# Kernel optimization log

Measured on AMD Instinct MI355X. Metric: run time of the kernel, lower is better.

The kernel has to match this reference:

```python
import jax, jax.numpy as jnp
import numpy as np

N, L, A, C, C2 = 10000, 5, 6, 20, 20

def setup_inputs() -> dict:
    key = jax.random.key(0)
    k1, k2, k3, k4 = jax.random.split(key, 4)
    stats = jax.random.uniform(k1, (N, L, A, C2), dtype=jnp.float32)
    layerS = jax.random.uniform(k2, (L,), dtype=jnp.float32)
    layerS = layerS / layerS.sum()
    arcS = jax.random.uniform(k3, (L, A), dtype=jnp.float32)
    arcS = arcS / arcS.sum(axis=1, keepdims=True)
    transition = jax.random.uniform(k4, (L, A, C, C2), dtype=jnp.float32)
    transition = transition / transition.sum(axis=2, keepdims=True)  # columns over C sum to 1
    return {"stats": stats, "layerS": layerS, "arcS": arcS, "transition": transition}

def reference(stats, layerS, arcS, transition):
    # neighbDim: [N,L,A,1,1]; zeros replaced by 1 to avoid div-by-zero
    neighbDim = stats.sum(axis=3, keepdims=True)[..., None]
    neighbDim = jnp.where(neighbDim == 0, jnp.float32(1.0), neighbDim)
    # rightmost_term: [N,L,A,C,C2]
    rightmost_term = transition[None, :, :, :, :] * stats[:, :, :, None, :] / neighbDim
    # tmp: [N,L,C] = sum over arcs of arcS * sum_{C2} rightmost
    tmp = (arcS[None, :, :, None] * rightmost_term.sum(axis=4)).sum(axis=2)
    # p_Q_given_obs: [N,C]
    p_Q_given_obs = (layerS[None, :, None] * tmp).sum(axis=1)
    # transition_posterior: [N,L,A,C,C2]
    transition_posterior = (layerS[None, :, None, None, None]
                            * arcS[None, :, :, None, None]
                            * rightmost_term)
    return (p_Q_given_obs, transition_posterior, rightmost_term)
```

## Files before the change

kernel.cpp:

```cpp
#include <hip/hip_runtime.h>
#include <hip/hip_bf16.h>


#define PQ_COUNT   200000
#define POST_OFF   200000
#define RT_OFF     (200000 + 120000000)

__global__ __launch_bounds__(256) void cgmm_kernel(
    const float* __restrict__ stats,
    const float* __restrict__ layerS,
    const float* __restrict__ arcS,
    const float* __restrict__ T,
    float* __restrict__ out)
{
    __shared__ __attribute__((aligned(16))) float s[600];
    __shared__ float invb[30];
    __shared__ float wgt[30];
    __shared__ float red[200];

    const int n = blockIdx.x;
    const int t = threadIdx.x;

    const float* sn = stats + (size_t)n * 600;
    for (int i = t; i < 600; i += 256) s[i] = sn[i];
    __syncthreads();

    if (t < 30) {
        float sum = 0.f;
        #pragma unroll
        for (int j = 0; j < 20; ++j) sum += s[t * 20 + j];
        invb[t] = (sum == 0.f) ? 1.f : 1.f / sum;
        wgt[t]  = layerS[t / 6] * arcS[t];
    }
    __syncthreads();

    const float4* T4 = (const float4*)T;
    const float4* s4 = (const float4*)s;
    float4* post4 = (float4*)(out + POST_OFF) + (size_t)n * 3000;
    float4* rt4o  = (float4*)(out + RT_OFF)   + (size_t)n * 3000;

    float acc = 0.f;
    if (t < 200) {
        const int r = t % 100;
        const int q = r % 5;
        #pragma unroll
        for (int pb = 0; pb < 30; pb += 2) {
            const int p = pb + t / 100;
            const float inv = invb[p];
            const float w   = wgt[p];
            const float4 tv = T4[p * 100 + r];
            const float4 sv = s4[p * 5 + q];
            float4 rt;
            rt.x = tv.x * sv.x * inv;
            rt.y = tv.y * sv.y * inv;
            rt.z = tv.z * sv.z * inv;
            rt.w = tv.w * sv.w * inv;
            float4 po;
            po.x = rt.x * w; po.y = rt.y * w;
            po.z = rt.z * w; po.w = rt.w * w;
            rt4o [p * 100 + r] = rt;
            post4[p * 100 + r] = po;
            acc += po.x + po.y + po.z + po.w;
        }
        red[t] = acc;
    }
    __syncthreads();

    if (t < 20) {
        float pq = 0.f;
        #pragma unroll
        for (int k = 0; k < 5; ++k)
            pq += red[t * 5 + k] + red[100 + t * 5 + k];
        out[(size_t)n * 20 + t] = pq;
    }
}

extern "C" void kernel_launch(void* const* d_in, const int* in_sizes, int n_in,
                              void* d_out, int out_size, void* d_ws, size_t ws_size,
                              hipStream_t stream) {
    const float* stats  = (const float*)d_in[0];
    const float* layerS = (const float*)d_in[1];
    const float* arcS   = (const float*)d_in[2];
    const float* T      = (const float*)d_in[3];
    float* out = (float*)d_out;
    cgmm_kernel<<<dim3(10000), dim3(256), 0, stream>>>(stats, layerS, arcS, T, out);
}
```

Measured before the change: 962.3 us.

## Split into reduction prep kernel and grid-stride streaming write kernel

Splits the single per-node kernel into two. A prep kernel computes inverse row sums, arc weights and p_Q_given_obs, and stores the inverses in workspace. A grid-stride streaming kernel then writes the two large output tensors with fully contiguous float4 stores spread over every thread. The aim is to stop 56 of each block's 256 threads idling during the dominant write phase and to make the stores more uniform. The cost is an extra launch, a second read of stats and T, and integer division per element. The original kernel is kept as a fallback when no workspace is available.

```diff
diff --git a/kernel.cpp b/kernel.cpp
--- a/kernel.cpp
+++ b/kernel.cpp
@@ -1,10 +1,112 @@
 #include <hip/hip_runtime.h>
-#include <hip/hip_bf16.h>
 
 
-#define PQ_COUNT   200000
-#define POST_OFF   200000
-#define RT_OFF     (200000 + 120000000)
+#define NN        10000
+#define POST_OFF  200000
+#define RT_OFF    (200000 + 120000000)
+#define TOTAL4    30000000
+
+__global__ __launch_bounds__(256) void cgmm_prep(
+    const float* __restrict__ stats,
+    const float* __restrict__ layerS,
+    const float* __restrict__ arcS,
+    const float* __restrict__ T,
+    float* __restrict__ out,
+    float* __restrict__ ws)
+{
+    __shared__ __attribute__((aligned(16))) float s[600];
+    __shared__ float invb[30];
+    __shared__ float wgt[30];
+    __shared__ float red[200];
+
+    const int n = blockIdx.x;
+    const int t = threadIdx.x;
+
+    const float* sn = stats + (size_t)n * 600;
+    for (int i = t; i < 600; i += 256) s[i] = sn[i];
+    __syncthreads();
+
+    if (t < 30) {
+        float sum = 0.f;
+        #pragma unroll
+        for (int j = 0; j < 20; ++j) sum += s[t * 20 + j];
+        const float iv = (sum == 0.f) ? 1.f : 1.f / sum;
+        invb[t] = iv;
+        ws[(size_t)n * 30 + t] = iv;
+        const float w = layerS[t / 6] * arcS[t];
+        wgt[t] = w;
+        if (n == 0) ws[(size_t)NN * 30 + t] = w;
+    }
+    __syncthreads();
+
+    const float4* T4 = (const float4*)T;
+    const float4* s4 = (const float4*)s;
+
+    float acc = 0.f;
+    if (t < 200) {
+        const int r = t % 100;
+        const int q = r % 5;
+        #pragma unroll
+        for (int pb = 0; pb < 30; pb += 2) {
+            const int p = pb + t / 100;
+            const float4 tv = T4[p * 100 + r];
+            const float4 sv = s4[p * 5 + q];
+            acc += (tv.x * sv.x + tv.y * sv.y + tv.z * sv.z + tv.w * sv.w)
+                   * (invb[p] * wgt[p]);
+        }
+        red[t] = acc;
+    }
+    __syncthreads();
+
+    if (t < 20) {
+        float pq = 0.f;
+        #pragma unroll
+        for (int k = 0; k < 5; ++k)
+            pq += red[t * 5 + k] + red[100 + t * 5 + k];
+        out[(size_t)n * 20 + t] = pq;
+    }
+}
+
+__global__ __launch_bounds__(256) void cgmm_stream(
+    const float* __restrict__ stats,
+    const float* __restrict__ T,
+    const float* __restrict__ ws,
+    float* __restrict__ out)
+{
+    const float4* T4 = (const float4*)T;
+    const float4* S4 = (const float4*)stats;
+    const float* invb = ws;
+    const float* wgt  = ws + (size_t)NN * 30;
+    float4* post4 = (float4*)(out + POST_OFF);
+    float4* rt4   = (float4*)(out + RT_OFF);
+
+    int idx = blockIdx.x * 256 + threadIdx.x;
+    const int stride = gridDim.x * 256;
+    for (; idx < TOTAL4; idx += stride) {
+        const int n   = idx / 3000;
+        const int rem = idx - n * 3000;
+        const int p   = rem / 100;
+        const int r   = rem - p * 100;
+        const int q   = r % 5;
+
+        const float4 tv = T4[rem];
+        const float4 sv = S4[(size_t)n * 150 + p * 5 + q];
+        const float iw  = invb[n * 30 + p];
+        const float w   = wgt[p];
+
+        float4 rt;
+        rt.x = tv.x * sv.x * iw;
+        rt.y = tv.y * sv.y * iw;
+        rt.z = tv.z * sv.z * iw;
+        rt.w = tv.w * sv.w * iw;
+        float4 po;
+        po.x = rt.x * w; po.y = rt.y * w;
+        po.z = rt.z * w; po.w = rt.w * w;
+
+        rt4[idx]   = rt;
+        post4[idx] = po;
+    }
+}
 
 __global__ __launch_bounds__(256) void cgmm_kernel(
     const float* __restrict__ stats,
@@ -83,5 +185,13 @@
     const float* arcS   = (const float*)d_in[2];
     const float* T      = (const float*)d_in[3];
     float* out = (float*)d_out;
-    cgmm_kernel<<<dim3(10000), dim3(256), 0, stream>>>(stats, layerS, arcS, T, out);
+
+    const size_t ws_need = (size_t)(NN * 30 + 30) * sizeof(float);
+    if (d_ws != nullptr && ws_size >= ws_need) {
+        float* ws = (float*)d_ws;
+        cgmm_prep  <<<dim3(NN),   dim3(256), 0, stream>>>(stats, layerS, arcS, T, out, ws);
+        cgmm_stream<<<dim3(2048), dim3(256), 0, stream>>>(stats, T, ws, out);
+    } else {
+        cgmm_kernel<<<dim3(NN), dim3(256), 0, stream>>>(stats, layerS, arcS, T, out);
+    }
 }
```

New measurement: 1.039 ms. +7.9%, slower.
